# Kernel tuning notes

Measured on AMD Instinct MI355X. Metric: run time of the kernel, lower is better.

Reference implementation:

```python
import jax, jax.numpy as jnp
import numpy as np

B, Q, C, N_PER, GS = 8, 2048, 256, 64, 8
H1, H2 = 256, 64
EPS = 1e-5


def make_grid():
    a = jnp.linspace(-0.1, 0.1, GS)
    gx, gy = jnp.meshgrid(a, a, indexing='ij')  # torch.meshgrid default 'ij'
    return jnp.stack([gx.reshape(-1), gy.reshape(-1)], axis=1)  # (n, 2)


def setup_inputs() -> dict:
    key = jax.random.key(0)
    ks = jax.random.split(key, 10)
    s = lambda k, shp, fan: jax.random.normal(k, shp, jnp.float32) / np.sqrt(fan)
    return {
        'tokens': jax.random.normal(ks[0], (B, Q, C), jnp.float32),
        'grid': make_grid(),
        'Wc': s(ks[1], (C, 3), C), 'bc': jnp.zeros((3,), jnp.float32),
        'W1': s(ks[2], (C + 2, H1), C + 2), 'b1': jnp.zeros((H1,), jnp.float32),
        'gamma1': jnp.ones((H1,), jnp.float32), 'beta1': jnp.zeros((H1,), jnp.float32),
        'W2': s(ks[3], (H1, H2), H1), 'b2': jnp.zeros((H2,), jnp.float32),
        'gamma2': jnp.ones((H2,), jnp.float32), 'beta2': jnp.zeros((H2,), jnp.float32),
        'W3': s(ks[4], (H2, 3), H2), 'b3': jnp.zeros((3,), jnp.float32),
    }


def batchnorm(x, gamma, beta):
    # BatchNorm1d in training mode: stats over batch (B*Q) and length (n) dims,
    # per channel (last axis here).
    mean = jnp.mean(x, axis=(0, 1, 2), keepdims=True)
    var = jnp.var(x, axis=(0, 1, 2), keepdims=True)
    return gamma * (x - mean) * jax.lax.rsqrt(var + EPS) + beta


def reference(tokens, grid, Wc, bc, W1, b1, gamma1, beta1, W2, b2, gamma2, beta2, W3, b3):
    coarse = tokens @ Wc + bc  # (B, Q, 3)
    # conv1 (1x1) on concat([tokens_expanded, grid]) == split matmul + broadcast add;
    # avoids materializing the (B,Q,n,C+2) concat explicitly.
    tok_part = tokens @ W1[:C]                 # (B, Q, H1)
    grid_part = grid @ W1[C:]                  # (n, H1)
    h = tok_part[:, :, None, :] + grid_part[None, None, :, :] + b1  # (B, Q, n, H1)
    h = jax.nn.relu(batchnorm(h, gamma1, beta1))
    h = jnp.einsum('bqnc,cd->bqnd', h, W2) + b2  # (B, Q, n, H2)
    h = jax.nn.relu(batchnorm(h, gamma2, beta2))
    disp = jnp.einsum('bqnc,cd->bqnd', h, W3) + b3  # (B, Q, n, 3)
    fine = (coarse[:, :, None, :] + disp).reshape(B, Q * N_PER, 3)
    return coarse, fine
```

## Files before the change

### kernel.cpp

```cpp
#include <hip/hip_runtime.h>
#include <hip/hip_bf16.h>

#define ROWS 16384
#define C_   256
#define H1_  256
#define H2_  64
#define EPSN 1e-5f

typedef __bf16 bf16x8 __attribute__((ext_vector_type(8)));
typedef __bf16 bf16x4 __attribute__((ext_vector_type(4)));
typedef __bf16 bf16x2 __attribute__((ext_vector_type(2)));
typedef float  f32x4  __attribute__((ext_vector_type(4)));
typedef float  f32x2  __attribute__((ext_vector_type(2)));

__device__ __forceinline__ bf16x2 cvt2(float a, float b) {
#if __has_builtin(__builtin_amdgcn_cvt_pk_bf16_f32)
    return __builtin_bit_cast(bf16x2, __builtin_amdgcn_cvt_pk_bf16_f32(a, b));
#else
    bf16x2 r; r[0] = (__bf16)a; r[1] = (__bf16)b; return r;
#endif
}

__global__ __launch_bounds__(256) void k0_pack(const float* __restrict__ W1,
                                               const float* __restrict__ W2,
                                               const float* __restrict__ W3,
                                               __bf16* __restrict__ W1p,
                                               __bf16* __restrict__ W2p,
                                               __bf16* __restrict__ W3p,
                                               float* __restrict__ zero_base) {
    int idx = blockIdx.x * 256 + threadIdx.x;
    if (idx < 65536) {
        int j = idx & 7, l = (idx >> 3) & 63, rest = idx >> 9;
        int ks = rest & 7, CT = rest >> 3;
        int k = ks * 32 + ((l >> 4) << 3) + j;
        int c = CT * 16 + (l & 15);
        W1p[idx] = (__bf16)W1[k * H1_ + c];
    } else {
        int i2 = idx - 65536;
        int j = i2 & 7, l = (i2 >> 3) & 63, rest = i2 >> 9;
        int ks = rest & 7, CK = rest >> 3;
        int k = ks * 32 + ((l >> 4) << 3) + j;
        int c2 = CK * 16 + (l & 15);
        W2p[i2] = (__bf16)W2[k * H2_ + c2];
    }
    if (idx < 1024) {
        int j = idx & 7, l = (idx >> 3) & 63, ks = idx >> 9;
        int k = ks * 32 + ((l >> 4) << 3) + j;
        int c = l & 15;
        W3p[idx] = (c < 3) ? (__bf16)W3[k * 3 + c] : (__bf16)0.f;
    }
    if (idx < 24576) zero_base[idx] = 0.0f;
}

__device__ __forceinline__ void prep_ctx(const float* __restrict__ grid,
                                         const float* __restrict__ W1,
                                         const float* __restrict__ a1p, int c0,
                                         f32x2* wgx2, f32x2* wgy2, float* A_) {
#pragma unroll
    for (int j = 0; j < 8; ++j) A_[j] = grid[2 * j + 1];
    f32x4 a0 = *(const f32x4*)(a1p + c0), a1h = *(const f32x4*)(a1p + c0 + 4);
    f32x4 x0 = *(const f32x4*)(W1 + C_ * H1_ + c0), x1 = *(const f32x4*)(W1 + C_ * H1_ + c0 + 4);
    f32x4 y0 = *(const f32x4*)(W1 + (C_ + 1) * H1_ + c0), yh = *(const f32x4*)(W1 + (C_ + 1) * H1_ + c0 + 4);
    float av[8] = {a0[0], a0[1], a0[2], a0[3], a1h[0], a1h[1], a1h[2], a1h[3]};
    float wx[8] = {x0[0], x0[1], x0[2], x0[3], x1[0], x1[1], x1[2], x1[3]};
    float wy[8] = {y0[0], y0[1], y0[2], y0[3], yh[0], yh[1], yh[2], yh[3]};
#pragma unroll
    for (int e = 0; e < 4; ++e) {
        wgx2[e][0] = av[2 * e] * wx[2 * e];     wgx2[e][1] = av[2 * e + 1] * wx[2 * e + 1];
        wgy2[e][0] = av[2 * e] * wy[2 * e];     wgy2[e][1] = av[2 * e + 1] * wy[2 * e + 1];
    }
}

__device__ __forceinline__ void stage16(__bf16* __restrict__ y1, int w, int c0, int nh,
                                        const float* __restrict__ a1p,
                                        const float* __restrict__ d1p,
                                        const f32x2* wgx2, const f32x2* wgy2,
                                        const float* A_,
                                        const float* __restrict__ tokrow) {
    f32x4 t0 = *(const f32x4*)(tokrow + c0);
    f32x4 t1 = *(const f32x4*)(tokrow + c0 + 4);
    f32x4 a0 = *(const f32x4*)(a1p + c0), a1h = *(const f32x4*)(a1p + c0 + 4);
    f32x4 d0 = *(const f32x4*)(d1p + c0), d1h = *(const f32x4*)(d1p + c0 + 4);
    f32x2 base2[4];
    base2[0][0] = fmaf(a0[0], t0[0], d0[0]);  base2[0][1] = fmaf(a0[1], t0[1], d0[1]);
    base2[1][0] = fmaf(a0[2], t0[2], d0[2]);  base2[1][1] = fmaf(a0[3], t0[3], d0[3]);
    base2[2][0] = fmaf(a1h[0], t1[0], d1h[0]); base2[2][1] = fmaf(a1h[1], t1[1], d1h[1]);
    base2[3][0] = fmaf(a1h[2], t1[2], d1h[2]); base2[3][1] = fmaf(a1h[3], t1[3], d1h[3]);
#pragma unroll
    for (int ih = 0; ih < 2; ++ih) {
        float axs = A_[2 * w + ih];
        f32x2 ax2 = {axs, axs};
        f32x2 tc2[4];
#pragma unroll
        for (int e = 0; e < 4; ++e) tc2[e] = __builtin_elementwise_fma(wgx2[e], ax2, base2[e]);
#pragma unroll
        for (int kk = 0; kk < 4; ++kk) {
            int iy = nh + 2 * kk;
            float ays = A_[iy];
            f32x2 ay2 = {ays, ays};
            f32x2 z = {0.f, 0.f};
            int n = w * 16 + ih * 8 + iy;
            bf16x8 out;
            bf16x2* o2 = (bf16x2*)&out;
#pragma unroll
            for (int e = 0; e < 4; ++e) {
                f32x2 v = __builtin_elementwise_max(
                    __builtin_elementwise_fma(wgy2[e], ay2, tc2[e]), z);
                o2[e] = cvt2(v[0], v[1]);
            }
            *(bf16x8*)(&y1[n * 264 + c0]) = out;
        }
    }
}

__global__ __launch_bounds__(256) void k1a(const float* __restrict__ tokens,
                                           const __bf16* __restrict__ W1p,
                                           const float* __restrict__ Wc,
                                           const float* __restrict__ bc,
                                           float* __restrict__ tokpart,
                                           float* __restrict__ coarse,
                                           float* __restrict__ p1s,
                                           float* __restrict__ p1q) {
    __shared__ __align__(16) __bf16 Al[16 * 264];
    int t = threadIdx.x, w = t >> 6, l = t & 63;
    int quad = l >> 4, col = l & 15;
    int rowbase = (blockIdx.x >> 1) * 16;
    int colhalf = blockIdx.x & 1;
    int slot = blockIdx.x & 31;

    bf16x8 bfr[16];
#pragma unroll
    for (int ctl = 0; ctl < 2; ++ctl)
#pragma unroll
        for (int ks = 0; ks < 8; ++ks) {
            int CT = colhalf * 8 + w * 2 + ctl;
            bfr[ctl * 8 + ks] = *(const bf16x8*)(W1p + (((CT * 8 + ks) * 64 + l) * 8));
        }
    {
        int r = t >> 4, cb = (t & 15) * 16;
        const float* src = tokens + (size_t)(rowbase + r) * C_ + cb;
        f32x4 t0 = *(const f32x4*)(src);
        f32x4 t1 = *(const f32x4*)(src + 4);
        f32x4 t2 = *(const f32x4*)(src + 8);
        f32x4 t3 = *(const f32x4*)(src + 12);
        bf16x8 v0, v1;
        bf16x2* p0 = (bf16x2*)&v0; bf16x2* p1 = (bf16x2*)&v1;
        p0[0] = cvt2(t0[0], t0[1]); p0[1] = cvt2(t0[2], t0[3]);
        p0[2] = cvt2(t1[0], t1[1]); p0[3] = cvt2(t1[2], t1[3]);
        p1[0] = cvt2(t2[0], t2[1]); p1[1] = cvt2(t2[2], t2[3]);
        p1[2] = cvt2(t3[0], t3[1]); p1[3] = cvt2(t3[2], t3[3]);
        *(bf16x8*)(&Al[r * 264 + cb]) = v0;
        *(bf16x8*)(&Al[r * 264 + cb + 8]) = v1;
    }
    __syncthreads();

    bf16x8 af[8];
#pragma unroll
    for (int ks = 0; ks < 8; ++ks)
        af[ks] = *(const bf16x8*)(&Al[col * 264 + ks * 32 + quad * 8]);

#pragma unroll
    for (int ctl = 0; ctl < 2; ++ctl) {
        f32x4 acc = {0.f, 0.f, 0.f, 0.f};
#pragma unroll
        for (int ks = 0; ks < 8; ++ks)
            acc = __builtin_amdgcn_mfma_f32_16x16x32_bf16(af[ks], bfr[ctl * 8 + ks], acc, 0, 0, 0);
        int c = colhalf * 128 + w * 32 + ctl * 16 + col;
        float s = 0.f, q = 0.f;
#pragma unroll
        for (int rr = 0; rr < 4; ++rr) {
            float v = acc[rr];
            tokpart[(size_t)(rowbase + quad * 4 + rr) * C_ + c] = v;
            s += v; q += v * v;
        }
        s += __shfl_xor(s, 16, 64); s += __shfl_xor(s, 32, 64);
        q += __shfl_xor(q, 16, 64); q += __shfl_xor(q, 32, 64);
        if (l < 16) {
            int cc = colhalf * 128 + w * 32 + ctl * 16 + l;
            atomicAdd(p1s + slot * C_ + cc, s);
            atomicAdd(p1q + slot * C_ + cc, q);
        }
    }
    if (colhalf == 0) {
        const f32x4* wcp = (const f32x4*)(Wc + l * 12);
        f32x4 wa = wcp[0], wb = wcp[1], wv = wcp[2];
        float wcl[12] = {wa[0], wa[1], wa[2], wa[3], wb[0], wb[1], wb[2], wb[3],
                         wv[0], wv[1], wv[2], wv[3]};
#pragma unroll
        for (int rr = 0; rr < 4; ++rr) {
            int r = w * 4 + rr;
            bf16x4 tv4 = *(const bf16x4*)(&Al[r * 264 + l * 4]);
            float p[3] = {0.f, 0.f, 0.f};
#pragma unroll
            for (int i = 0; i < 4; ++i) {
                float tvf = (float)tv4[i];
#pragma unroll
                for (int j = 0; j < 3; ++j) p[j] = fmaf(tvf, wcl[i * 3 + j], p[j]);
            }
#pragma unroll
            for (int off = 1; off < 64; off <<= 1)
#pragma unroll
                for (int j = 0; j < 3; ++j) p[j] += __shfl_xor(p[j], off, 64);
            if (l == 0) {
#pragma unroll
                for (int j = 0; j < 3; ++j)
                    coarse[(size_t)(rowbase + r) * 3 + j] = p[j] + bc[j];
            }
        }
    }
}

__global__ void k1b(const float* __restrict__ grid, const float* __restrict__ W1,
                    const float* __restrict__ gamma1, const float* __restrict__ beta1,
                    const float* __restrict__ p1s, const float* __restrict__ p1q,
                    float* __restrict__ a1o, float* __restrict__ d1o) {
    int t = threadIdx.x;
    float S = 0.f, Qq = 0.f;
    for (int s = 0; s < 32; ++s) { S += p1s[s * C_ + t]; Qq += p1q[s * C_ + t]; }
    float mean_t = S / (float)ROWS;
    float var_t = Qq / (float)ROWS - mean_t * mean_t;
    float wx = W1[C_ * H1_ + t];
    float wy = W1[(C_ + 1) * H1_ + t];
    float mg = 0.f, qg = 0.f;
    for (int n = 0; n < 64; ++n) {
        float gv = grid[2 * n] * wx + grid[2 * n + 1] * wy;
        mg += gv; qg += gv * gv;
    }
    mg *= (1.f / 64.f);
    float var_g = qg * (1.f / 64.f) - mg * mg;
    float a1 = gamma1[t] * rsqrtf(var_t + var_g + EPSN);
    a1o[t] = a1;
    d1o[t] = beta1[t] - a1 * (mean_t + mg);
}

template <bool SPILL>
__global__ __launch_bounds__(256) void k2(const float* __restrict__ tokpart,
                                          const float* __restrict__ grid,
                                          const float* __restrict__ W1,
                                          const __bf16* __restrict__ W2p,
                                          const float* __restrict__ a1,
                                          const float* __restrict__ d1,
                                          float* __restrict__ p2s,
                                          float* __restrict__ p2q,
                                          __bf16* __restrict__ h2s) {
    __shared__ __align__(16) __bf16 y1[64 * 264];
    __shared__ __align__(16) __bf16 y2l[SPILL ? 64 * 72 : 8];
    int t = threadIdx.x, w = t >> 6, l = t & 63;
    int quad = l >> 4, col = l & 15;
    int wn = w >> 1, wc = w & 1;
    int c0 = (l & 31) * 8, nh = l >> 5;

    bf16x8 bfr[16];
#pragma unroll
    for (int ck = 0; ck < 2; ++ck)
#pragma unroll
        for (int ks = 0; ks < 8; ++ks)
            bfr[ck * 8 + ks] = *(const bf16x8*)(W2p + ((((wc * 2 + ck) * 8 + ks) * 64 + l) * 8));

    f32x2 wgx2[4], wgy2[4]; float A_[8];
    prep_ctx(grid, W1, a1, c0, wgx2, wgy2, A_);

    float s[2][4] = {}, q[2][4] = {};

#pragma unroll 1
    for (int r8 = 0; r8 < 8; ++r8) {
        int row = blockIdx.x * 8 + r8;
        stage16(y1, w, c0, nh, a1, d1, wgx2, wgy2, A_, tokpart + (size_t)row * C_);
        __syncthreads();
#pragma unroll
        for (int rt = 0; rt < 2; ++rt) {
            bf16x8 af[8];
#pragma unroll
            for (int ks = 0; ks < 8; ++ks)
                af[ks] = *(const bf16x8*)(&y1[(wn * 32 + rt * 16 + col) * 264 + ks * 32 + quad * 8]);
#pragma unroll
            for (int ck = 0; ck < 2; ++ck) {
                f32x4 acc = {0.f, 0.f, 0.f, 0.f};
#pragma unroll
                for (int ks = 0; ks < 8; ++ks)
                    acc = __builtin_amdgcn_mfma_f32_16x16x32_bf16(bfr[ck * 8 + ks], af[ks], acc, 0, 0, 0);
#pragma unroll
                for (int rr = 0; rr < 4; ++rr) {
                    s[ck][rr] += acc[rr];
                    q[ck][rr] += acc[rr] * acc[rr];
                }
                if constexpr (SPILL) {
                    bf16x4 v; bf16x2* v2 = (bf16x2*)&v;
                    v2[0] = cvt2(acc[0], acc[1]);
                    v2[1] = cvt2(acc[2], acc[3]);
                    *(bf16x4*)(&y2l[(wn * 32 + rt * 16 + col) * 72 + wc * 32 + ck * 16 + quad * 4]) = v;
                }
            }
        }
        __syncthreads();
        if constexpr (SPILL) {
            int n = t >> 2, cb = (t & 3) * 16;
            bf16x8 u0 = *(const bf16x8*)(&y2l[n * 72 + cb]);
            bf16x8 u1 = *(const bf16x8*)(&y2l[n * 72 + cb + 8]);
            __bf16* dst = h2s + (size_t)row * 4096 + t * 16;
            *(bf16x8*)dst = u0;
            *(bf16x8*)(dst + 8) = u1;
        }
    }
    int slot = blockIdx.x & 63;
#pragma unroll
    for (int ck = 0; ck < 2; ++ck)
#pragma unroll
        for (int rr = 0; rr < 4; ++rr) {
            float sv = s[ck][rr], qv = q[ck][rr];
            sv += __shfl_xor(sv, 1, 64); sv += __shfl_xor(sv, 2, 64);
            sv += __shfl_xor(sv, 4, 64); sv += __shfl_xor(sv, 8, 64);
            qv += __shfl_xor(qv, 1, 64); qv += __shfl_xor(qv, 2, 64);
            qv += __shfl_xor(qv, 4, 64); qv += __shfl_xor(qv, 8, 64);
            if (col == 0) {
                int c2 = wc * 32 + ck * 16 + quad * 4 + rr;
                atomicAdd(p2s + slot * H2_ + c2, sv);
                atomicAdd(p2q + slot * H2_ + c2, qv);
            }
        }
}

__global__ void k2b(const float* __restrict__ p2s, const float* __restrict__ p2q,
                    const float* __restrict__ gamma2, const float* __restrict__ beta2,
                    float* __restrict__ a2o, float* __restrict__ d2o) {
    int t = threadIdx.x;
    float S = 0.f, Qq = 0.f;
    for (int s = 0; s < 64; ++s) { S += p2s[s * H2_ + t]; Qq += p2q[s * H2_ + t]; }
    const float invN = 1.f / ((float)ROWS * 64.f);
    float mean = S * invN;
    float var = Qq * invN - mean * mean;
    float a2 = gamma2[t] * rsqrtf(var + EPSN);
    a2o[t] = a2;
    d2o[t] = beta2[t] - a2 * mean;
}

__global__ __launch_bounds__(256) void k3s(const __bf16* __restrict__ h2s,
                                           const float* __restrict__ a2,
                                           const float* __restrict__ d2p,
                                           const __bf16* __restrict__ W3p,
                                           const float* __restrict__ b3,
                                           const float* __restrict__ coarse,
                                           float* __restrict__ fine) {
    __shared__ __align__(16) __bf16 y2l[8][64 * 72];
    __shared__ __align__(16) float finebuf[8 * 192];
    int t = threadIdx.x, w = t >> 6, l = t & 63;
    int quad = l >> 4, col = l & 15;

    bf16x8 wfr[2];
#pragma unroll
    for (int ks = 0; ks < 2; ++ks)
        wfr[ks] = *(const bf16x8*)(W3p + ((ks * 64 + l) * 8));

    int n = t >> 2, cb = (t & 3) * 16;
    float a2r[16], d2r[16];
#pragma unroll
    for (int i = 0; i < 16; i += 4) {
        f32x4 av = *(const f32x4*)(a2 + cb + i);
        f32x4 dv = *(const f32x4*)(d2p + cb + i);
#pragma unroll
        for (int e = 0; e < 4; ++e) { a2r[i + e] = av[e]; d2r[i + e] = dv[e]; }
    }
#pragma unroll 1
    for (int r8 = 0; r8 < 8; ++r8) {
        size_t row = (size_t)blockIdx.x * 8 + r8;
        const __bf16* src = h2s + row * 4096 + t * 16;
        bf16x8 u0 = *(const bf16x8*)src;
        bf16x8 u1 = *(const bf16x8*)(src + 8);
        bf16x8 o0, o1;
        bf16x2* p0 = (bf16x2*)&o0; bf16x2* p1 = (bf16x2*)&o1;
#pragma unroll
        for (int e = 0; e < 4; ++e) {
            p0[e] = cvt2(fmaxf(fmaf(a2r[2 * e],     (float)u0[2 * e],     d2r[2 * e]), 0.f),
                         fmaxf(fmaf(a2r[2 * e + 1], (float)u0[2 * e + 1], d2r[2 * e + 1]), 0.f));
            p1[e] = cvt2(fmaxf(fmaf(a2r[8 + 2 * e],     (float)u1[2 * e],     d2r[8 + 2 * e]), 0.f),
                         fmaxf(fmaf(a2r[8 + 2 * e + 1], (float)u1[2 * e + 1], d2r[8 + 2 * e + 1]), 0.f));
        }
        *(bf16x8*)(&y2l[r8][n * 72 + cb]) = o0;
        *(bf16x8*)(&y2l[r8][n * 72 + cb + 8]) = o1;
    }
    __syncthreads();
    float b3v = (col < 3) ? b3[col] : 0.f;
#pragma unroll 1
    for (int r8 = 0; r8 < 8; ++r8) {
        int row = blockIdx.x * 8 + r8;
        bf16x8 af2[2];
#pragma unroll
        for (int ks = 0; ks < 2; ++ks)
            af2[ks] = *(const bf16x8*)(&y2l[r8][(w * 16 + col) * 72 + ks * 32 + quad * 8]);
        f32x4 acc = {0.f, 0.f, 0.f, 0.f};
        acc = __builtin_amdgcn_mfma_f32_16x16x32_bf16(af2[0], wfr[0], acc, 0, 0, 0);
        acc = __builtin_amdgcn_mfma_f32_16x16x32_bf16(af2[1], wfr[1], acc, 0, 0, 0);
        if (col < 3) {
            float cj = coarse[row * 3 + col] + b3v;
#pragma unroll
            for (int rr = 0; rr < 4; ++rr)
                finebuf[r8 * 192 + (w * 16 + quad * 4 + rr) * 3 + col] = acc[rr] + cj;
        }
    }
    __syncthreads();
    {
        float* dst = fine + (size_t)blockIdx.x * 1536;
        const f32x4* fb = (const f32x4*)finebuf;
        *(f32x4*)(dst + 4 * t) = fb[t];
        if (t < 128) *(f32x4*)(dst + 1024 + 4 * t) = fb[256 + t];
    }
}

__global__ __launch_bounds__(256) void k3r(const float* __restrict__ tokpart,
                                           const float* __restrict__ grid,
                                           const float* __restrict__ W1,
                                           const __bf16* __restrict__ W2p,
                                           const float* __restrict__ a1,
                                           const float* __restrict__ d1,
                                           const __bf16* __restrict__ W3p,
                                           const float* __restrict__ a2,
                                           const float* __restrict__ d2p,
                                           const float* __restrict__ b3,
                                           const float* __restrict__ coarse,
                                           float* __restrict__ fine) {
    __shared__ __align__(16) __bf16 y1[64 * 264];
    __shared__ __align__(16) __bf16 y2l[64 * 72];
    __shared__ __align__(16) float finebuf[8 * 192];
    int t = threadIdx.x, w = t >> 6, l = t & 63;
    int quad = l >> 4, col = l & 15;
    int wn = w >> 1, wc = w & 1;
    int c0 = (l & 31) * 8, nh = l >> 5;

    bf16x8 bfr[16];
#pragma unroll
    for (int ck = 0; ck < 2; ++ck)
#pragma unroll
        for (int ks = 0; ks < 8; ++ks)
            bfr[ck * 8 + ks] = *(const bf16x8*)(W2p + ((((wc * 2 + ck) * 8 + ks) * 64 + l) * 8));
    bf16x8 wfr[2];
#pragma unroll
    for (int ks = 0; ks < 2; ++ks)
        wfr[ks] = *(const bf16x8*)(W3p + ((ks * 64 + l) * 8));

    f32x2 wgx2[4], wgy2[4]; float A_[8];
    prep_ctx(grid, W1, a1, c0, wgx2, wgy2, A_);

    float a2v[8], d2v[8];
#pragma unroll
    for (int ck = 0; ck < 2; ++ck)
#pragma unroll
        for (int rr = 0; rr < 4; ++rr) {
            int c2 = wc * 32 + ck * 16 + quad * 4 + rr;
            a2v[ck * 4 + rr] = a2[c2];
            d2v[ck * 4 + rr] = d2p[c2];
        }
    float b3v = (col < 3) ? b3[col] : 0.f;

#pragma unroll 1
    for (int r8 = 0; r8 < 8; ++r8) {
        int row = blockIdx.x * 8 + r8;
        stage16(y1, w, c0, nh, a1, d1, wgx2, wgy2, A_, tokpart + (size_t)row * C_);
        __syncthreads();
#pragma unroll
        for (int rt = 0; rt < 2; ++rt) {
            bf16x8 af[8];
#pragma unroll
            for (int ks = 0; ks < 8; ++ks)
                af[ks] = *(const bf16x8*)(&y1[(wn * 32 + rt * 16 + col) * 264 + ks * 32 + quad * 8]);
#pragma unroll
            for (int ck = 0; ck < 2; ++ck) {
                f32x4 acc = {0.f, 0.f, 0.f, 0.f};
#pragma unroll
                for (int ks = 0; ks < 8; ++ks)
                    acc = __builtin_amdgcn_mfma_f32_16x16x32_bf16(bfr[ck * 8 + ks], af[ks], acc, 0, 0, 0);
                bf16x4 v; bf16x2* v2 = (bf16x2*)&v;
                float y0 = fmaxf(fmaf(a2v[ck * 4 + 0], acc[0], d2v[ck * 4 + 0]), 0.f);
                float y1v = fmaxf(fmaf(a2v[ck * 4 + 1], acc[1], d2v[ck * 4 + 1]), 0.f);
                float y2 = fmaxf(fmaf(a2v[ck * 4 + 2], acc[2], d2v[ck * 4 + 2]), 0.f);
                float y3 = fmaxf(fmaf(a2v[ck * 4 + 3], acc[3], d2v[ck * 4 + 3]), 0.f);
                v2[0] = cvt2(y0, y1v); v2[1] = cvt2(y2, y3);
                *(bf16x4*)(&y2l[(wn * 32 + rt * 16 + col) * 72 + wc * 32 + ck * 16 + quad * 4]) = v;
            }
        }
        __syncthreads();
        bf16x8 af2[2];
#pragma unroll
        for (int ks = 0; ks < 2; ++ks)
            af2[ks] = *(const bf16x8*)(&y2l[(w * 16 + col) * 72 + ks * 32 + quad * 8]);
        f32x4 d2acc = {0.f, 0.f, 0.f, 0.f};
        d2acc = __builtin_amdgcn_mfma_f32_16x16x32_bf16(af2[0], wfr[0], d2acc, 0, 0, 0);
        d2acc = __builtin_amdgcn_mfma_f32_16x16x32_bf16(af2[1], wfr[1], d2acc, 0, 0, 0);
        if (col < 3) {
            float cj = coarse[row * 3 + col] + b3v;
#pragma unroll
            for (int rr = 0; rr < 4; ++rr)
                finebuf[r8 * 192 + (w * 16 + quad * 4 + rr) * 3 + col] = d2acc[rr] + cj;
        }
    }
    __syncthreads();
    {
        float* dst = fine + (size_t)blockIdx.x * 1536;
        const f32x4* fb = (const f32x4*)finebuf;
        *(f32x4*)(dst + 4 * t) = fb[t];
        if (t < 128) *(f32x4*)(dst + 1024 + 4 * t) = fb[256 + t];
    }
}

extern "C" void kernel_launch(void* const* d_in, const int* in_sizes, int n_in,
                              void* d_out, int out_size, void* d_ws, size_t ws_size,
                              hipStream_t stream) {
    (void)in_sizes; (void)n_in; (void)out_size;
    const float* tokens = (const float*)d_in[0];
    const float* grid   = (const float*)d_in[1];
    const float* Wc     = (const float*)d_in[2];
    const float* bc     = (const float*)d_in[3];
    const float* W1     = (const float*)d_in[4];
    const float* gamma1 = (const float*)d_in[6];
    const float* beta1  = (const float*)d_in[7];
    const float* W2     = (const float*)d_in[8];
    const float* gamma2 = (const float*)d_in[10];
    const float* beta2  = (const float*)d_in[11];
    const float* W3     = (const float*)d_in[12];
    const float* b3     = (const float*)d_in[13];

    char* ws = (char*)d_ws;
    __bf16* W1p     = (__bf16*)(ws);
    __bf16* W2p     = (__bf16*)(ws + 131072);
    float*  p1s     = (float*)(ws + 163840);
    float*  p1q     = (float*)(ws + 196608);
    float*  p2s     = (float*)(ws + 229376);
    float*  p2q     = (float*)(ws + 245760);
    float*  a1      = (float*)(ws + 262144);
    float*  d1      = (float*)(ws + 263168);
    float*  a2      = (float*)(ws + 264192);
    float*  d2p     = (float*)(ws + 264448);
    __bf16* W3p     = (__bf16*)(ws + 264704);
    float*  tokpart = (float*)(ws + 266752);
    __bf16* h2s     = (__bf16*)(ws + 17043968);

    const size_t SPILL_NEED = 17043968ull + 134217728ull;
    bool spill = ws_size >= SPILL_NEED;

    float* coarse = (float*)d_out;
    float* fine   = (float*)d_out + (size_t)ROWS * 3;

    k0_pack<<<320, 256, 0, stream>>>(W1, W2, W3, W1p, W2p, W3p, p1s);
    k1a<<<2048, 256, 0, stream>>>(tokens, W1p, Wc, bc, tokpart, coarse, p1s, p1q);
    k1b<<<1, 256, 0, stream>>>(grid, W1, gamma1, beta1, p1s, p1q, a1, d1);
    if (spill) {
        k2<true><<<ROWS / 8, 256, 0, stream>>>(tokpart, grid, W1, W2p, a1, d1, p2s, p2q, h2s);
        k2b<<<1, 64, 0, stream>>>(p2s, p2q, gamma2, beta2, a2, d2p);
        k3s<<<ROWS / 8, 256, 0, stream>>>(h2s, a2, d2p, W3p, b3, coarse, fine);
    } else {
        k2<false><<<ROWS / 8, 256, 0, stream>>>(tokpart, grid, W1, W2p, a1, d1, p2s, p2q, h2s);
        k2b<<<1, 64, 0, stream>>>(p2s, p2q, gamma2, beta2, a2, d2p);
        k3r<<<ROWS / 8, 256, 0, stream>>>(tokpart, grid, W1, W2p, a1, d1, W3p, a2, d2p, b3, coarse, fine);
    }
}
```

Before: 212.4 us.

## Split layer-2 channels across blocks and store h2 in MFMA fragment layout

The spill-path layer-2 kernel now launches twice as many blocks. Each block computes half of the 64 output channels, and each wave handles its own 16 points, so the two block-wide barriers and the LDS transpose buffer are gone. The bf16 intermediate is written straight from MFMA accumulators in a layout that the final kernel reads directly, so k3s also drops its LDS staging and barrier. The cost is that every block repeats the layer-1 BN/ReLU staging for its rows, doubling that work, and the global stores become smaller 8-byte writes. The non-spill path keeps the old kernel as k2f.

Measured after the change: 239.2 us. 12.6% more time.

```diff
diff --git a/kernel.cpp b/kernel.cpp
--- a/kernel.cpp
+++ b/kernel.cpp
@@ -233,91 +233,76 @@
     d1o[t] = beta1[t] - a1 * (mean_t + mg);
 }
 
-template <bool SPILL>
-__global__ __launch_bounds__(256) void k2(const float* __restrict__ tokpart,
-                                          const float* __restrict__ grid,
-                                          const float* __restrict__ W1,
-                                          const __bf16* __restrict__ W2p,
-                                          const float* __restrict__ a1,
-                                          const float* __restrict__ d1,
-                                          float* __restrict__ p2s,
-                                          float* __restrict__ p2q,
-                                          __bf16* __restrict__ h2s) {
+__global__ __launch_bounds__(256) void k2n(const float* __restrict__ tokpart,
+                                           const float* __restrict__ grid,
+                                           const float* __restrict__ W1,
+                                           const __bf16* __restrict__ W2p,
+                                           const float* __restrict__ a1,
+                                           const float* __restrict__ d1,
+                                           float* __restrict__ p2s,
+                                           float* __restrict__ p2q,
+                                           __bf16* __restrict__ h2s) {
     __shared__ __align__(16) __bf16 y1[64 * 264];
-    __shared__ __align__(16) __bf16 y2l[SPILL ? 64 * 72 : 8];
     int t = threadIdx.x, w = t >> 6, l = t & 63;
     int quad = l >> 4, col = l & 15;
-    int wn = w >> 1, wc = w & 1;
     int c0 = (l & 31) * 8, nh = l >> 5;
+    int rowgrp = blockIdx.x >> 1;
+    int ch2 = blockIdx.x & 1;
 
     bf16x8 bfr[16];
 #pragma unroll
     for (int ck = 0; ck < 2; ++ck)
 #pragma unroll
-        for (int ks = 0; ks < 8; ++ks)
-            bfr[ck * 8 + ks] = *(const bf16x8*)(W2p + ((((wc * 2 + ck) * 8 + ks) * 64 + l) * 8));
+        for (int ks = 0; ks < 8; ++ks) {
+            int CK = ch2 * 2 + ck;
+            bfr[ck * 8 + ks] = *(const bf16x8*)(W2p + (((CK * 8 + ks) * 64 + l) * 8));
+        }
 
     f32x2 wgx2[4], wgy2[4]; float A_[8];
     prep_ctx(grid, W1, a1, c0, wgx2, wgy2, A_);
 
-    float s[2][4] = {}, q[2][4] = {};
+    float s[8] = {}, q[8] = {};
 
 #pragma unroll 1
     for (int r8 = 0; r8 < 8; ++r8) {
-        int row = blockIdx.x * 8 + r8;
+        int row = rowgrp * 8 + r8;
         stage16(y1, w, c0, nh, a1, d1, wgx2, wgy2, A_, tokpart + (size_t)row * C_);
-        __syncthreads();
-#pragma unroll
-        for (int rt = 0; rt < 2; ++rt) {
-            bf16x8 af[8];
+        bf16x8 af[8];
+#pragma unroll
+        for (int ks = 0; ks < 8; ++ks)
+            af[ks] = *(const bf16x8*)(&y1[(w * 16 + col) * 264 + ks * 32 + quad * 8]);
+        __bf16* dst = h2s + (((size_t)row * 64 + w * 16 + col) * 64 + ch2 * 32 + quad * 4);
+#pragma unroll
+        for (int ck = 0; ck < 2; ++ck) {
+            f32x4 acc = {0.f, 0.f, 0.f, 0.f};
 #pragma unroll
             for (int ks = 0; ks < 8; ++ks)
-                af[ks] = *(const bf16x8*)(&y1[(wn * 32 + rt * 16 + col) * 264 + ks * 32 + quad * 8]);
-#pragma unroll
-            for (int ck = 0; ck < 2; ++ck) {
-                f32x4 acc = {0.f, 0.f, 0.f, 0.f};
-#pragma unroll
-                for (int ks = 0; ks < 8; ++ks)
-                    acc = __builtin_amdgcn_mfma_f32_16x16x32_bf16(bfr[ck * 8 + ks], af[ks], acc, 0, 0, 0);
-#pragma unroll
-                for (int rr = 0; rr < 4; ++rr) {
-                    s[ck][rr] += acc[rr];
-                    q[ck][rr] += acc[rr] * acc[rr];
-                }
-                if constexpr (SPILL) {
-                    bf16x4 v; bf16x2* v2 = (bf16x2*)&v;
-                    v2[0] = cvt2(acc[0], acc[1]);
-                    v2[1] = cvt2(acc[2], acc[3]);
-                    *(bf16x4*)(&y2l[(wn * 32 + rt * 16 + col) * 72 + wc * 32 + ck * 16 + quad * 4]) = v;
-                }
-            }
-        }
-        __syncthreads();
-        if constexpr (SPILL) {
-            int n = t >> 2, cb = (t & 3) * 16;
-            bf16x8 u0 = *(const bf16x8*)(&y2l[n * 72 + cb]);
-            bf16x8 u1 = *(const bf16x8*)(&y2l[n * 72 + cb + 8]);
-            __bf16* dst = h2s + (size_t)row * 4096 + t * 16;
-            *(bf16x8*)dst = u0;
-            *(bf16x8*)(dst + 8) = u1;
+                acc = __builtin_amdgcn_mfma_f32_16x16x32_bf16(bfr[ck * 8 + ks], af[ks], acc, 0, 0, 0);
+#pragma unroll
+            for (int rr = 0; rr < 4; ++rr) {
+                s[ck * 4 + rr] += acc[rr];
+                q[ck * 4 + rr] = fmaf(acc[rr], acc[rr], q[ck * 4 + rr]);
+            }
+            bf16x4 v; bf16x2* v2 = (bf16x2*)&v;
+            v2[0] = cvt2(acc[0], acc[1]);
+            v2[1] = cvt2(acc[2], acc[3]);
+            *(bf16x4*)(dst + ck * 16) = v;
         }
     }
     int slot = blockIdx.x & 63;
 #pragma unroll
-    for (int ck = 0; ck < 2; ++ck)
-#pragma unroll
-        for (int rr = 0; rr < 4; ++rr) {
-            float sv = s[ck][rr], qv = q[ck][rr];
-            sv += __shfl_xor(sv, 1, 64); sv += __shfl_xor(sv, 2, 64);
-            sv += __shfl_xor(sv, 4, 64); sv += __shfl_xor(sv, 8, 64);
-            qv += __shfl_xor(qv, 1, 64); qv += __shfl_xor(qv, 2, 64);
-            qv += __shfl_xor(qv, 4, 64); qv += __shfl_xor(qv, 8, 64);
-            if (col == 0) {
-                int c2 = wc * 32 + ck * 16 + quad * 4 + rr;
-                atomicAdd(p2s + slot * H2_ + c2, sv);
-                atomicAdd(p2q + slot * H2_ + c2, qv);
-            }
-        }
+    for (int i = 0; i < 8; ++i) {
+        float sv = s[i], qv = q[i];
+        sv += __shfl_xor(sv, 1, 64); sv += __shfl_xor(sv, 2, 64);
+        sv += __shfl_xor(sv, 4, 64); sv += __shfl_xor(sv, 8, 64);
+        qv += __shfl_xor(qv, 1, 64); qv += __shfl_xor(qv, 2, 64);
+        qv += __shfl_xor(qv, 4, 64); qv += __shfl_xor(qv, 8, 64);
+        if (col == 0) {
+            int c2 = ch2 * 32 + (i >> 2) * 16 + quad * 4 + (i & 3);
+            atomicAdd(p2s + slot * H2_ + c2, sv);
+            atomicAdd(p2q + slot * H2_ + c2, qv);
+        }
+    }
 }
 
 __global__ void k2b(const float* __restrict__ p2s, const float* __restrict__ p2q,
@@ -341,7 +326,6 @@
                                            const float* __restrict__ b3,
                                            const float* __restrict__ coarse,
                                            float* __restrict__ fine) {
-    __shared__ __align__(16) __bf16 y2l[8][64 * 72];
     __shared__ __align__(16) float finebuf[8 * 192];
     int t = threadIdx.x, w = t >> 6, l = t & 63;
     int quad = l >> 4, col = l & 15;
@@ -351,45 +335,39 @@
     for (int ks = 0; ks < 2; ++ks)
         wfr[ks] = *(const bf16x8*)(W3p + ((ks * 64 + l) * 8));
 
-    int n = t >> 2, cb = (t & 3) * 16;
     float a2r[16], d2r[16];
 #pragma unroll
-    for (int i = 0; i < 16; i += 4) {
-        f32x4 av = *(const f32x4*)(a2 + cb + i);
-        f32x4 dv = *(const f32x4*)(d2p + cb + i);
-#pragma unroll
-        for (int e = 0; e < 4; ++e) { a2r[i + e] = av[e]; d2r[i + e] = dv[e]; }
-    }
-#pragma unroll 1
-    for (int r8 = 0; r8 < 8; ++r8) {
-        size_t row = (size_t)blockIdx.x * 8 + r8;
-        const __bf16* src = h2s + row * 4096 + t * 16;
-        bf16x8 u0 = *(const bf16x8*)src;
-        bf16x8 u1 = *(const bf16x8*)(src + 8);
-        bf16x8 o0, o1;
-        bf16x2* p0 = (bf16x2*)&o0; bf16x2* p1 = (bf16x2*)&o1;
+    for (int h = 0; h < 2; ++h) {
+        f32x4 av0 = *(const f32x4*)(a2 + h * 32 + quad * 8);
+        f32x4 av1 = *(const f32x4*)(a2 + h * 32 + quad * 8 + 4);
+        f32x4 dv0 = *(const f32x4*)(d2p + h * 32 + quad * 8);
+        f32x4 dv1 = *(const f32x4*)(d2p + h * 32 + quad * 8 + 4);
 #pragma unroll
         for (int e = 0; e < 4; ++e) {
-            p0[e] = cvt2(fmaxf(fmaf(a2r[2 * e],     (float)u0[2 * e],     d2r[2 * e]), 0.f),
-                         fmaxf(fmaf(a2r[2 * e + 1], (float)u0[2 * e + 1], d2r[2 * e + 1]), 0.f));
-            p1[e] = cvt2(fmaxf(fmaf(a2r[8 + 2 * e],     (float)u1[2 * e],     d2r[8 + 2 * e]), 0.f),
-                         fmaxf(fmaf(a2r[8 + 2 * e + 1], (float)u1[2 * e + 1], d2r[8 + 2 * e + 1]), 0.f));
-        }
-        *(bf16x8*)(&y2l[r8][n * 72 + cb]) = o0;
-        *(bf16x8*)(&y2l[r8][n * 72 + cb + 8]) = o1;
-    }
-    __syncthreads();
+            a2r[h * 8 + e] = av0[e]; a2r[h * 8 + 4 + e] = av1[e];
+            d2r[h * 8 + e] = dv0[e]; d2r[h * 8 + 4 + e] = dv1[e];
+        }
+    }
     float b3v = (col < 3) ? b3[col] : 0.f;
+
 #pragma unroll 1
     for (int r8 = 0; r8 < 8; ++r8) {
         int row = blockIdx.x * 8 + r8;
-        bf16x8 af2[2];
-#pragma unroll
-        for (int ks = 0; ks < 2; ++ks)
-            af2[ks] = *(const bf16x8*)(&y2l[r8][(w * 16 + col) * 72 + ks * 32 + quad * 8]);
+        const __bf16* src = h2s + (((size_t)row * 64 + w * 16 + col) * 64 + quad * 8);
+        bf16x8 u0 = *(const bf16x8*)src;
+        bf16x8 u1 = *(const bf16x8*)(src + 32);
+        bf16x8 f0, f1;
+        bf16x2* g0 = (bf16x2*)&f0; bf16x2* g1 = (bf16x2*)&f1;
+#pragma unroll
+        for (int e = 0; e < 4; ++e) {
+            g0[e] = cvt2(fmaxf(fmaf(a2r[2 * e],     (float)u0[2 * e],     d2r[2 * e]), 0.f),
+                         fmaxf(fmaf(a2r[2 * e + 1], (float)u0[2 * e + 1], d2r[2 * e + 1]), 0.f));
+            g1[e] = cvt2(fmaxf(fmaf(a2r[8 + 2 * e],     (float)u1[2 * e],     d2r[8 + 2 * e]), 0.f),
+                         fmaxf(fmaf(a2r[8 + 2 * e + 1], (float)u1[2 * e + 1], d2r[8 + 2 * e + 1]), 0.f));
+        }
         f32x4 acc = {0.f, 0.f, 0.f, 0.f};
-        acc = __builtin_amdgcn_mfma_f32_16x16x32_bf16(af2[0], wfr[0], acc, 0, 0, 0);
-        acc = __builtin_amdgcn_mfma_f32_16x16x32_bf16(af2[1], wfr[1], acc, 0, 0, 0);
+        acc = __builtin_amdgcn_mfma_f32_16x16x32_bf16(f0, wfr[0], acc, 0, 0, 0);
+        acc = __builtin_amdgcn_mfma_f32_16x16x32_bf16(f1, wfr[1], acc, 0, 0, 0);
         if (col < 3) {
             float cj = coarse[row * 3 + col] + b3v;
 #pragma unroll
@@ -404,6 +382,72 @@
         *(f32x4*)(dst + 4 * t) = fb[t];
         if (t < 128) *(f32x4*)(dst + 1024 + 4 * t) = fb[256 + t];
     }
+}
+
+__global__ __launch_bounds__(256) void k2f(const float* __restrict__ tokpart,
+                                           const float* __restrict__ grid,
+                                           const float* __restrict__ W1,
+                                           const __bf16* __restrict__ W2p,
+                                           const float* __restrict__ a1,
+                                           const float* __restrict__ d1,
+                                           float* __restrict__ p2s,
+                                           float* __restrict__ p2q) {
+    __shared__ __align__(16) __bf16 y1[64 * 264];
+    int t = threadIdx.x, w = t >> 6, l = t & 63;
+    int quad = l >> 4, col = l & 15;
+    int wn = w >> 1, wc = w & 1;
+    int c0 = (l & 31) * 8, nh = l >> 5;
+    bf16x8 bfr[16];
+#pragma unroll
+    for (int ck = 0; ck < 2; ++ck)
+#pragma unroll
+        for (int ks = 0; ks < 8; ++ks)
+            bfr[ck * 8 + ks] = *(const bf16x8*)(W2p + ((((wc * 2 + ck) * 8 + ks) * 64 + l) * 8));
+    f32x2 wgx2[4], wgy2[4]; float A_[8];
+    prep_ctx(grid, W1, a1, c0, wgx2, wgy2, A_);
+    float s[2][4] = {}, q[2][4] = {};
+#pragma unroll 1
+    for (int r8 = 0; r8 < 8; ++r8) {
+        int row = blockIdx.x * 8 + r8;
+        stage16(y1, w, c0, nh, a1, d1, wgx2, wgy2, A_, tokpart + (size_t)row * C_);
+        __syncthreads();
+#pragma unroll
+        for (int rt = 0; rt < 2; ++rt) {
+            bf16x8 af[8];
+#pragma unroll
+            for (int ks = 0; ks < 8; ++ks)
+                af[ks] = *(const bf16x8*)(&y1[(wn * 32 + rt * 16 + col) * 264 + ks * 32 + quad * 8]);
+#pragma unroll
+            for (int ck = 0; ck < 2; ++ck) {
+                f32x4 acc = {0.f, 0.f, 0.f, 0.f};
+#pragma unroll
+                for (int ks = 0; ks < 8; ++ks)
+                    acc = __builtin_amdgcn_mfma_f32_16x16x32_bf16(bfr[ck * 8 + ks], af[ks], acc, 0, 0, 0);
+#pragma unroll
+                for (int rr = 0; rr < 4; ++rr) {
+                    s[ck][rr] += acc[rr];
+                    q[ck][rr] = fmaf(acc[rr], acc[rr], q[ck][rr]);
+                }
+            }
+        }
+        __syncthreads();
+    }
+    int slot = blockIdx.x & 63;
+#pragma unroll
+    for (int ck = 0; ck < 2; ++ck)
+#pragma unroll
+        for (int rr = 0; rr < 4; ++rr) {
+            float sv = s[ck][rr], qv = q[ck][rr];
+            sv += __shfl_xor(sv, 1, 64); sv += __shfl_xor(sv, 2, 64);
+            sv += __shfl_xor(sv, 4, 64); sv += __shfl_xor(sv, 8, 64);
+            qv += __shfl_xor(qv, 1, 64); qv += __shfl_xor(qv, 2, 64);
+            qv += __shfl_xor(qv, 4, 64); qv += __shfl_xor(qv, 8, 64);
+            if (col == 0) {
+                int c2 = wc * 32 + ck * 16 + quad * 4 + rr;
+                atomicAdd(p2s + slot * H2_ + c2, sv);
+                atomicAdd(p2q + slot * H2_ + c2, qv);
+            }
+        }
 }
 
 __global__ __launch_bounds__(256) void k3r(const float* __restrict__ tokpart,
@@ -425,7 +469,6 @@
     int quad = l >> 4, col = l & 15;
     int wn = w >> 1, wc = w & 1;
     int c0 = (l & 31) * 8, nh = l >> 5;
-
     bf16x8 bfr[16];
 #pragma unroll
     for (int ck = 0; ck < 2; ++ck)
@@ -436,10 +479,8 @@
 #pragma unroll
     for (int ks = 0; ks < 2; ++ks)
         wfr[ks] = *(const bf16x8*)(W3p + ((ks * 64 + l) * 8));
-
     f32x2 wgx2[4], wgy2[4]; float A_[8];
     prep_ctx(grid, W1, a1, c0, wgx2, wgy2, A_);
-
     float a2v[8], d2v[8];
 #pragma unroll
     for (int ck = 0; ck < 2; ++ck)
@@ -450,7 +491,6 @@
             d2v[ck * 4 + rr] = d2p[c2];
         }
     float b3v = (col < 3) ? b3[col] : 0.f;
-
 #pragma unroll 1
     for (int r8 = 0; r8 < 8; ++r8) {
         int row = blockIdx.x * 8 + r8;
@@ -543,11 +583,11 @@
     k1a<<<2048, 256, 0, stream>>>(tokens, W1p, Wc, bc, tokpart, coarse, p1s, p1q);
     k1b<<<1, 256, 0, stream>>>(grid, W1, gamma1, beta1, p1s, p1q, a1, d1);
     if (spill) {
-        k2<true><<<ROWS / 8, 256, 0, stream>>>(tokpart, grid, W1, W2p, a1, d1, p2s, p2q, h2s);
+        k2n<<<ROWS / 8 * 2, 256, 0, stream>>>(tokpart, grid, W1, W2p, a1, d1, p2s, p2q, h2s);
         k2b<<<1, 64, 0, stream>>>(p2s, p2q, gamma2, beta2, a2, d2p);
         k3s<<<ROWS / 8, 256, 0, stream>>>(h2s, a2, d2p, W3p, b3, coarse, fine);
     } else {
-        k2<false><<<ROWS / 8, 256, 0, stream>>>(tokpart, grid, W1, W2p, a1, d1, p2s, p2q, h2s);
+        k2f<<<ROWS / 8, 256, 0, stream>>>(tokpart, grid, W1, W2p, a1, d1, p2s, p2q);
         k2b<<<1, 64, 0, stream>>>(p2s, p2q, gamma2, beta2, a2, d2p);
         k3r<<<ROWS / 8, 256, 0, stream>>>(tokpart, grid, W1, W2p, a1, d1, W3p, a2, d2p, b3, coarse, fine);
     }
```
